# Optimization experiments

Measured on AMD Instinct MI355X. Metric: run time of the kernel, lower is better.

## Reference

```python
import jax, jax.numpy as jnp
import numpy as np

D_MODEL = 1024
N_HEADS = 16
D_K = D_MODEL // N_HEADS
LN_EPS = 1e-5


def setup_inputs() -> dict:
    key = jax.random.key(0)
    ks = jax.random.split(key, 8)
    B, Sq, Skv = 2, 2048, 2048
    scale = 1.0 / np.sqrt(D_MODEL)
    return {
        "query": jax.random.normal(ks[0], (B, Sq, D_MODEL), dtype=jnp.float32),
        "key_value": jax.random.normal(ks[1], (B, Skv, D_MODEL), dtype=jnp.float32),
        "W_qkv": jax.random.normal(ks[2], (3 * D_MODEL, D_MODEL), dtype=jnp.float32) * scale,
        "b_qkv": jax.random.normal(ks[3], (3 * D_MODEL,), dtype=jnp.float32) * 0.01,
        "W_o": jax.random.normal(ks[4], (D_MODEL, D_MODEL), dtype=jnp.float32) * scale,
        "b_o": jax.random.normal(ks[5], (D_MODEL,), dtype=jnp.float32) * 0.01,
        "ln_gamma": jnp.ones((D_MODEL,), dtype=jnp.float32),
        "ln_beta": jnp.zeros((D_MODEL,), dtype=jnp.float32),
    }


def _attention(query, key_value, W_qkv, b_qkv, W_o, b_o, ln_gamma, ln_beta):
    B, Sq, _ = query.shape
    Skv = key_value.shape[1]
    # Q from query rows of qkv_proj; K,V from key_value rows (slice weights -> same
    # math as projecting then slicing, without the discarded 2/3 and 1/3 compute).
    Wq, Wk, Wv = W_qkv[:D_MODEL], W_qkv[D_MODEL:2 * D_MODEL], W_qkv[2 * D_MODEL:]
    bq, bk, bv = b_qkv[:D_MODEL], b_qkv[D_MODEL:2 * D_MODEL], b_qkv[2 * D_MODEL:]
    Q = (query @ Wq.T + bq).reshape(B, Sq, N_HEADS, D_K).transpose(0, 2, 1, 3)
    K = (key_value @ Wk.T + bk).reshape(B, Skv, N_HEADS, D_K).transpose(0, 2, 1, 3)
    V = (key_value @ Wv.T + bv).reshape(B, Skv, N_HEADS, D_K).transpose(0, 2, 1, 3)
    # fp32 attention (original forces float32 inside autocast(enabled=False))
    scores = jnp.einsum('bhqd,bhkd->bhqk', Q.astype(jnp.float32), K.astype(jnp.float32))
    scores = scores / np.sqrt(D_K)
    attn = jax.nn.softmax(scores, axis=-1)  # dropout is identity at inference
    context = jnp.einsum('bhqk,bhkd->bhqd', attn, V.astype(jnp.float32)).astype(query.dtype)
    context = context.transpose(0, 2, 1, 3).reshape(B, Sq, D_MODEL)
    output = context @ W_o.T + b_o
    # residual + LayerNorm
    x = output + query
    mu = jnp.mean(x, axis=-1, keepdims=True)
    var = jnp.mean(jnp.square(x - mu), axis=-1, keepdims=True)
    return (x - mu) / jnp.sqrt(var + LN_EPS) * ln_gamma + ln_beta


def reference(query, key_value, W_qkv, b_qkv, W_o, b_o, ln_gamma, ln_beta):
    return _attention(query, key_value, W_qkv, b_qkv, W_o, b_o, ln_gamma, ln_beta)
```

## Files before the change

### kernel.cpp

```cpp
#include <hip/hip_runtime.h>
#include <hip/hip_bf16.h>

typedef __attribute__((ext_vector_type(4))) float f32x4;
typedef __attribute__((ext_vector_type(16))) float f32x16;
typedef __attribute__((ext_vector_type(8))) __bf16 bf16x8;
typedef __attribute__((ext_vector_type(2))) __bf16 bf16x2;

#define DEV __device__ __forceinline__

DEV unsigned short f2bf(float f) {
    union { float f; unsigned u; } x; x.f = f;
    unsigned r = x.u + 0x7fffu + ((x.u >> 16) & 1u);
    return (unsigned short)(r >> 16);
}

DEV unsigned packbf(float a, float b) {
    union { bf16x2 h; unsigned u; } t;
    t.h[0] = (__bf16)a; t.h[1] = (__bf16)b;
    return t.u;
}

DEV float bflo(unsigned u) { union { unsigned u; float f; } x; x.u = u << 16; return x.f; }
DEV float bfhi(unsigned u) { union { unsigned u; float f; } x; x.u = u & 0xffff0000u; return x.f; }

DEV void gload16(const void* g, void* l) {
    __builtin_amdgcn_global_load_lds(
        (const __attribute__((address_space(1))) void*)g,
        (__attribute__((address_space(3))) void*)l, 16, 0, 0);
}

#define PLSWAP(a, b) asm("v_permlane32_swap_b32 %0, %1" : "+v"(a), "+v"(b))

DEV bf16x8 ldsfrag(const unsigned short* base, int row, int kcol) {
    int byte = (row << 7) + (kcol << 1);
    byte ^= (row & 7) << 4;
    return *reinterpret_cast<const bf16x8*>(reinterpret_cast<const char*>(base) + byte);
}

__global__ __launch_bounds__(256) void cvt_all(
    const float* __restrict__ q, const float* __restrict__ kv,
    const float* __restrict__ wq, const float* __restrict__ wo,
    unsigned short* __restrict__ qb, unsigned short* __restrict__ kvb,
    unsigned short* __restrict__ wqb, unsigned short* __restrict__ wob)
{
    int i = blockIdx.x * 256 + threadIdx.x;
    const float* s; unsigned short* d; int o;
    if (i < 2097152) {
        if (i < 1048576) { s = q;  d = qb;  o = i; }
        else             { s = kv; d = kvb; o = i - 1048576; }
    } else {
        if (i < 2883584) { s = wq; d = wqb; o = i - 2097152; }
        else             { s = wo; d = wob; o = i - 2883584; }
    }
    f32x4 v = *reinterpret_cast<const f32x4*>(s + (size_t)o * 4);
    ushort4 u;
    u.x = f2bf(v.x); u.y = f2bf(v.y); u.z = f2bf(v.z); u.w = f2bf(v.w);
    *reinterpret_cast<ushort4*>(d + (size_t)o * 4) = u;
}

__global__ __launch_bounds__(256) void gemm_qkv(
    const unsigned short* __restrict__ Aq,
    const unsigned short* __restrict__ Akv,
    const unsigned short* __restrict__ W,
    const float* __restrict__ bias,
    unsigned short* __restrict__ QP,
    unsigned short* __restrict__ KP,
    unsigned short* __restrict__ VP)
{
    __shared__ unsigned short lA[2][128 * 64];
    __shared__ unsigned short lB[2][128 * 64];
    int bn = blockIdx.x % 24, bm = blockIdx.x / 24;
    int m0 = bm * 128, n0 = bn * 128;
    const unsigned short* A = (bn < 8) ? Aq : Akv;
    int tid = threadIdx.x, lane = tid & 63, wv = tid >> 6;
    int wm = (wv >> 1) * 64, wn = (wv & 1) * 64;
    int cg = lane >> 4, cl = lane & 15;

    const unsigned short* sA[4];
    const unsigned short* sB[4];
#pragma unroll
    for (int p = 0; p < 4; ++p) {
        int o = p * 4096 + tid * 16;
        int r = o >> 7;
        int c = ((o ^ ((r & 7) << 4)) >> 1) & 63;
        sA[p] = A + (size_t)(m0 + r) * 1024 + c;
        sB[p] = W + (size_t)(n0 + r) * 1024 + c;
    }
    const int dl = wv * 1024;

    auto STAGE = [&](int buf, int k0) {
#pragma unroll
        for (int p = 0; p < 4; ++p) {
            gload16(sA[p] + k0, (char*)lA[buf] + p * 4096 + dl);
            gload16(sB[p] + k0, (char*)lB[buf] + p * 4096 + dl);
        }
    };

    f32x4 acc[4][4] = {};

    STAGE(0, 0);
    for (int kt = 0; kt < 16; ++kt) {
        const int cur = kt & 1;
        if (kt < 15) {
            STAGE(cur ^ 1, (kt + 1) * 64);
            asm volatile("s_waitcnt vmcnt(8)" ::: "memory");
        } else {
            asm volatile("s_waitcnt vmcnt(0)" ::: "memory");
        }
        __builtin_amdgcn_s_barrier();
#pragma unroll
        for (int ks = 0; ks < 2; ++ks) {
            bf16x8 af[4], bfr[4];
#pragma unroll
            for (int i = 0; i < 4; ++i) af[i] = ldsfrag(lA[cur], wm + i * 16 + cl, ks * 32 + cg * 8);
#pragma unroll
            for (int j = 0; j < 4; ++j) bfr[j] = ldsfrag(lB[cur], wn + j * 16 + cl, ks * 32 + cg * 8);
#pragma unroll
            for (int i = 0; i < 4; ++i)
#pragma unroll
                for (int j = 0; j < 4; ++j)
                    acc[i][j] = __builtin_amdgcn_mfma_f32_16x16x32_bf16(af[i], bfr[j], acc[i][j], 0, 0, 0);
        }
        asm volatile("s_waitcnt lgkmcnt(0)" ::: "memory");
        __builtin_amdgcn_s_barrier();
    }

    unsigned short* img = (unsigned short*)lA;
    const int which = (bn >= 16) ? 2 : (bn >= 8 ? 1 : 0);
    const float scale = (which == 0) ? 0.18033688f : 1.0f;

#pragma unroll
    for (int j = 0; j < 4; ++j) {
        int nn = wn + j * 16 + cl;
        int d = nn & 63, chunk = nn >> 6;
        float bv = bias[n0 + nn];
#pragma unroll
        for (int i = 0; i < 4; ++i) {
#pragma unroll
            for (int r = 0; r < 4; ++r) {
                int mm = wm + i * 16 + cg * 4 + r;
                float v = (acc[i][j][r] + bv) * scale;
                int off;
                if (which < 2)
                    off = ((mm >> 5) * 4 + (d >> 4)) * 512
                        + (((d >> 3) & 1) * 32 + (mm & 31)) * 8 + (d & 7);
                else
                    off = (((mm >> 6) * 2 + (d >> 5)) * 4 + ((mm >> 4) & 3)) * 512
                        + (((mm >> 3) & 1) * 32 + (d & 31)) * 8 + (mm & 7);
                img[chunk * 8192 + off] = f2bf(v);
            }
        }
    }
    __syncthreads();

    int bb = m0 >> 11, s0 = m0 & 2047;
    int h0 = (bn & 7) * 2;
    unsigned short* dst[2];
#pragma unroll
    for (int c = 0; c < 2; ++c) {
        int bh = bb * 16 + h0 + c;
        if (which == 0)      dst[c] = QP + ((size_t)bh * 64 + (s0 >> 5)) * 2048;
        else if (which == 1) dst[c] = KP + ((size_t)bh * 64 + (s0 >> 5)) * 2048;
        else                 dst[c] = VP + ((size_t)bh * 32 + (s0 >> 6)) * 4096;
    }
#pragma unroll
    for (int c = 0; c < 2; ++c)
#pragma unroll
        for (int k = 0; k < 4; ++k) {
            int e = (k * 256 + tid) * 8;
            *reinterpret_cast<uint4*>(dst[c] + e) =
                *reinterpret_cast<const uint4*>(img + c * 8192 + e);
        }
}

__global__ __launch_bounds__(256, 2) void attn(
    const unsigned short* __restrict__ QP,
    const unsigned short* __restrict__ KP,
    const unsigned short* __restrict__ VP,
    unsigned short* __restrict__ OP,
    float2* __restrict__ ML)
{
    int swz = (blockIdx.x & 7) * 64 + (blockIdx.x >> 3);
    int bh = swz >> 4;
    int qc = (swz >> 1) & 7;
    int spl = swz & 1;
    int tid = threadIdx.x, lane = tid & 63, wv = tid >> 6;
    int ql = lane & 31, hh = lane >> 5;
    int qs = qc * 256 + wv * 64;
    const unsigned short* kp = KP + (size_t)bh * 131072 + lane * 8;
    const unsigned short* vp = VP + (size_t)bh * 131072 + lane * 8;
    const int tbase = spl * 16;

    bf16x8 qfA[4], qfB[4];
    {
        const unsigned short* qpA = QP + ((size_t)(bh * 64 + (qs >> 5)) * 4) * 512 + lane * 8;
#pragma unroll
        for (int ks = 0; ks < 4; ++ks) {
            qfA[ks] = *reinterpret_cast<const bf16x8*>(qpA + ks * 512);
            qfB[ks] = *reinterpret_cast<const bf16x8*>(qpA + 2048 + ks * 512);
        }
    }

    bf16x8 ka[4], kc[4], va[4], vc[4];
    auto LOADK = [&](int t) {
        const unsigned short* b = kp + (size_t)t * 4096;
#pragma unroll
        for (int ks = 0; ks < 4; ++ks) {
            ka[ks] = *reinterpret_cast<const bf16x8*>(b + ks * 512);
            kc[ks] = *reinterpret_cast<const bf16x8*>(b + 2048 + ks * 512);
        }
    };
    auto LOADV = [&](int t) {
        const unsigned short* b = vp + (size_t)t * 4096;
#pragma unroll
        for (int kh = 0; kh < 4; ++kh) {
            va[kh] = *reinterpret_cast<const bf16x8*>(b + kh * 512);
            vc[kh] = *reinterpret_cast<const bf16x8*>(b + 2048 + kh * 512);
        }
    };

    f32x16 oA0 = {}, oA1 = {}, oB0 = {}, oB1 = {};
    f32x4 psA = {0.f, 0.f, 0.f, 0.f}, psB = {0.f, 0.f, 0.f, 0.f};

    auto EXPPACK = [&](f32x16& s0, f32x16& s1, unsigned (&pb)[4][4], f32x4& psa) {
#pragma unroll
        for (int r = 0; r < 16; r += 4) {
            s0[r]     = __builtin_amdgcn_exp2f(s0[r]);     psa[0] += s0[r];
            s0[r + 1] = __builtin_amdgcn_exp2f(s0[r + 1]); psa[1] += s0[r + 1];
            s0[r + 2] = __builtin_amdgcn_exp2f(s0[r + 2]); psa[2] += s0[r + 2];
            s0[r + 3] = __builtin_amdgcn_exp2f(s0[r + 3]); psa[3] += s0[r + 3];
        }
#pragma unroll
        for (int r = 0; r < 16; r += 4) {
            s1[r]     = __builtin_amdgcn_exp2f(s1[r]);     psa[0] += s1[r];
            s1[r + 1] = __builtin_amdgcn_exp2f(s1[r + 1]); psa[1] += s1[r + 1];
            s1[r + 2] = __builtin_amdgcn_exp2f(s1[r + 2]); psa[2] += s1[r + 2];
            s1[r + 3] = __builtin_amdgcn_exp2f(s1[r + 3]); psa[3] += s1[r + 3];
        }
        unsigned A0 = packbf(s0[0], s0[1]),   B0 = packbf(s0[2], s0[3]);
        unsigned C0 = packbf(s0[4], s0[5]),   D0 = packbf(s0[6], s0[7]);
        unsigned E0 = packbf(s0[8], s0[9]),   F0 = packbf(s0[10], s0[11]);
        unsigned G0 = packbf(s0[12], s0[13]), H0 = packbf(s0[14], s0[15]);
        unsigned A1 = packbf(s1[0], s1[1]),   B1 = packbf(s1[2], s1[3]);
        unsigned C1 = packbf(s1[4], s1[5]),   D1 = packbf(s1[6], s1[7]);
        unsigned E1 = packbf(s1[8], s1[9]),   F1 = packbf(s1[10], s1[11]);
        unsigned G1 = packbf(s1[12], s1[13]), H1 = packbf(s1[14], s1[15]);
        PLSWAP(A0, C0); PLSWAP(B0, D0); PLSWAP(E0, G0); PLSWAP(F0, H0);
        PLSWAP(A1, C1); PLSWAP(B1, D1); PLSWAP(E1, G1); PLSWAP(F1, H1);
        pb[0][0] = A0; pb[0][1] = B0; pb[0][2] = C0; pb[0][3] = D0;
        pb[1][0] = E0; pb[1][1] = F0; pb[1][2] = G0; pb[1][3] = H0;
        pb[2][0] = A1; pb[2][1] = B1; pb[2][2] = C1; pb[2][3] = D1;
        pb[3][0] = E1; pb[3][1] = F1; pb[3][2] = G1; pb[3][3] = H1;
    };

    LOADK(tbase);
    LOADV(tbase);
    for (int t = 0; t < 16; ++t) {
        f32x16 sA0 = {}, sA1 = {};
        __builtin_amdgcn_s_setprio(1);
#pragma unroll
        for (int ks = 0; ks < 4; ++ks) {
            sA0 = __builtin_amdgcn_mfma_f32_32x32x16_bf16(ka[ks], qfA[ks], sA0, 0, 0, 0);
            sA1 = __builtin_amdgcn_mfma_f32_32x32x16_bf16(kc[ks], qfA[ks], sA1, 0, 0, 0);
        }
        __builtin_amdgcn_s_setprio(0);
        unsigned pbA[4][4];
        EXPPACK(sA0, sA1, pbA, psA);
        f32x16 sB0 = {}, sB1 = {};
        __builtin_amdgcn_s_setprio(1);
#pragma unroll
        for (int ks = 0; ks < 4; ++ks) {
            sB0 = __builtin_amdgcn_mfma_f32_32x32x16_bf16(ka[ks], qfB[ks], sB0, 0, 0, 0);
            sB1 = __builtin_amdgcn_mfma_f32_32x32x16_bf16(kc[ks], qfB[ks], sB1, 0, 0, 0);
        }
        __builtin_amdgcn_s_setprio(0);
        LOADK(tbase + t + 1);
        __builtin_amdgcn_s_setprio(1);
#pragma unroll
        for (int kh = 0; kh < 4; ++kh) {
            union { unsigned u[4]; bf16x8 v; } pa;
            pa.u[0] = pbA[kh][0]; pa.u[1] = pbA[kh][1];
            pa.u[2] = pbA[kh][2]; pa.u[3] = pbA[kh][3];
            oA0 = __builtin_amdgcn_mfma_f32_32x32x16_bf16(va[kh], pa.v, oA0, 0, 0, 0);
            oA1 = __builtin_amdgcn_mfma_f32_32x32x16_bf16(vc[kh], pa.v, oA1, 0, 0, 0);
        }
        __builtin_amdgcn_s_setprio(0);
        unsigned pbB[4][4];
        EXPPACK(sB0, sB1, pbB, psB);
        __builtin_amdgcn_s_setprio(1);
#pragma unroll
        for (int kh = 0; kh < 4; ++kh) {
            union { unsigned u[4]; bf16x8 v; } pc;
            pc.u[0] = pbB[kh][0]; pc.u[1] = pbB[kh][1];
            pc.u[2] = pbB[kh][2]; pc.u[3] = pbB[kh][3];
            oB0 = __builtin_amdgcn_mfma_f32_32x32x16_bf16(va[kh], pc.v, oB0, 0, 0, 0);
            oB1 = __builtin_amdgcn_mfma_f32_32x32x16_bf16(vc[kh], pc.v, oB1, 0, 0, 0);
        }
        __builtin_amdgcn_s_setprio(0);
        LOADV(tbase + t + 1);
    }

    float lA = (psA[0] + psA[1]) + (psA[2] + psA[3]);
    float lB = (psB[0] + psB[1]) + (psB[2] + psB[3]);
    float lAx = lA, lBx = lB;
    PLSWAP(lA, lAx); PLSWAP(lB, lBx);
    lA += lAx; lB += lBx;

    size_t rowA = (size_t)(spl * 32 + bh) * 2048 + qs + ql;
    size_t rowB = rowA + 32;
    if (hh == 0) {
        ML[rowA] = make_float2(0.0f, lA);
        ML[rowB] = make_float2(0.0f, lB);
    }
    float invA = 1.0f / lA, invB = 1.0f / lB;
    unsigned short* cpA = OP + rowA * 64 + hh * 4;
    unsigned short* cpB = OP + rowB * 64 + hh * 4;
#pragma unroll
    for (int m = 0; m < 4; ++m) {
        uint2 w0, w1;
        w0.x = packbf(oA0[4 * m] * invA, oA0[4 * m + 1] * invA);
        w0.y = packbf(oA0[4 * m + 2] * invA, oA0[4 * m + 3] * invA);
        w1.x = packbf(oA1[4 * m] * invA, oA1[4 * m + 1] * invA);
        w1.y = packbf(oA1[4 * m + 2] * invA, oA1[4 * m + 3] * invA);
        *reinterpret_cast<uint2*>(cpA + 8 * m) = w0;
        *reinterpret_cast<uint2*>(cpA + 32 + 8 * m) = w1;
        w0.x = packbf(oB0[4 * m] * invB, oB0[4 * m + 1] * invB);
        w0.y = packbf(oB0[4 * m + 2] * invB, oB0[4 * m + 3] * invB);
        w1.x = packbf(oB1[4 * m] * invB, oB1[4 * m + 1] * invB);
        w1.y = packbf(oB1[4 * m + 2] * invB, oB1[4 * m + 3] * invB);
        *reinterpret_cast<uint2*>(cpB + 8 * m) = w0;
        *reinterpret_cast<uint2*>(cpB + 32 + 8 * m) = w1;
    }
}

__global__ __launch_bounds__(256) void combine(
    const unsigned short* __restrict__ OP,
    const float2* __restrict__ ML,
    unsigned short* __restrict__ ctx)
{
    int row = blockIdx.x * 256 + threadIdx.x;
    int bh = row >> 11, q = row & 2047;
    float2 ml1 = ML[row];
    float2 ml2 = ML[65536 + row];
    float M = fmaxf(ml1.x, ml2.x);
    float w1 = ml1.y * __builtin_amdgcn_exp2f(ml1.x - M);
    float w2 = ml2.y * __builtin_amdgcn_exp2f(ml2.x - M);
    float inv = 1.0f / (w1 + w2);
    w1 *= inv; w2 *= inv;
    const unsigned short* p1 = OP + (size_t)row * 64;
    const unsigned short* p2 = OP + ((size_t)65536 + row) * 64;
    int b = bh >> 4, h = bh & 15;
    unsigned short* op = ctx + (size_t)(b * 2048 + q) * 1024 + h * 64;
#pragma unroll
    for (int c = 0; c < 8; ++c) {
        uint4 u1 = *reinterpret_cast<const uint4*>(p1 + c * 8);
        uint4 u2 = *reinterpret_cast<const uint4*>(p2 + c * 8);
        uint4 r;
        r.x = packbf(bflo(u1.x) * w1 + bflo(u2.x) * w2, bfhi(u1.x) * w1 + bfhi(u2.x) * w2);
        r.y = packbf(bflo(u1.y) * w1 + bflo(u2.y) * w2, bfhi(u1.y) * w1 + bfhi(u2.y) * w2);
        r.z = packbf(bflo(u1.z) * w1 + bflo(u2.z) * w2, bfhi(u1.z) * w1 + bfhi(u2.z) * w2);
        r.w = packbf(bflo(u1.w) * w1 + bflo(u2.w) * w2, bfhi(u1.w) * w1 + bfhi(u2.w) * w2);
        *reinterpret_cast<uint4*>(op + c * 8) = r;
    }
}

__global__ __launch_bounds__(256) void gemm_out(
    const unsigned short* __restrict__ A,
    const unsigned short* __restrict__ W,
    const float* __restrict__ bo,
    const float* __restrict__ resid,
    float* __restrict__ X)
{
    __shared__ unsigned short lA[3][64 * 64];
    __shared__ unsigned short lB[3][128 * 64];
    int bn = blockIdx.x & 7, bm = blockIdx.x >> 3;
    int m0 = bm * 64, n0 = bn * 128;
    int tid = threadIdx.x, lane = tid & 63, wv = tid >> 6;
    int wm = (wv >> 1) * 32, wn = (wv & 1) * 64;
    int cg = lane >> 4, cl = lane & 15;

    const unsigned short* sA[2];
    const unsigned short* sB[4];
#pragma unroll
    for (int p = 0; p < 2; ++p) {
        int o = p * 4096 + tid * 16;
        int r = o >> 7;
        int c = ((o ^ ((r & 7) << 4)) >> 1) & 63;
        sA[p] = A + (size_t)(m0 + r) * 1024 + c;
    }
#pragma unroll
    for (int p = 0; p < 4; ++p) {
        int o = p * 4096 + tid * 16;
        int r = o >> 7;
        int c = ((o ^ ((r & 7) << 4)) >> 1) & 63;
        sB[p] = W + (size_t)(n0 + r) * 1024 + c;
    }
    const int dl = wv * 1024;

    auto STAGE = [&](int buf, int k0) {
#pragma unroll
        for (int p = 0; p < 2; ++p)
            gload16(sA[p] + k0, (char*)lA[buf] + p * 4096 + dl);
#pragma unroll
        for (int p = 0; p < 4; ++p)
            gload16(sB[p] + k0, (char*)lB[buf] + p * 4096 + dl);
    };

    f32x4 acc[2][4] = {};

    STAGE(0, 0);
    STAGE(1, 64);
    int cur = 0;
    for (int kt = 0; kt < 16; ++kt) {
        __builtin_amdgcn_s_barrier();
        if (kt < 14) {
            int nb = (cur >= 1) ? cur - 1 : 2;
            STAGE(nb, (kt + 2) * 64);
            asm volatile("s_waitcnt vmcnt(12)" ::: "memory");
        } else if (kt == 14) {
            asm volatile("s_waitcnt vmcnt(6)" ::: "memory");
        } else {
            asm volatile("s_waitcnt vmcnt(0)" ::: "memory");
        }
#pragma unroll
        for (int ks = 0; ks < 2; ++ks) {
            bf16x8 af[2], bfr[4];
#pragma unroll
            for (int i = 0; i < 2; ++i) af[i] = ldsfrag(lA[cur], wm + i * 16 + cl, ks * 32 + cg * 8);
#pragma unroll
            for (int j = 0; j < 4; ++j) bfr[j] = ldsfrag(lB[cur], wn + j * 16 + cl, ks * 32 + cg * 8);
#pragma unroll
            for (int i = 0; i < 2; ++i)
#pragma unroll
                for (int j = 0; j < 4; ++j)
                    acc[i][j] = __builtin_amdgcn_mfma_f32_16x16x32_bf16(af[i], bfr[j], acc[i][j], 0, 0, 0);
        }
        cur = (cur == 2) ? 0 : cur + 1;
    }

#pragma unroll
    for (int j = 0; j < 4; ++j) {
        int n = n0 + wn + j * 16 + cl;
        float bv = bo[n];
#pragma unroll
        for (int i = 0; i < 2; ++i)
#pragma unroll
            for (int r = 0; r < 4; ++r) {
                int m = m0 + wm + i * 16 + cg * 4 + r;
                size_t idx = (size_t)m * 1024 + n;
                X[idx] = acc[i][j][r] + bv + resid[idx];
            }
    }
}

__global__ __launch_bounds__(256) void ln_k(float* __restrict__ X,
                                            const float* __restrict__ gam,
                                            const float* __restrict__ bet)
{
    __shared__ float red[8];
    int row = blockIdx.x, tid = threadIdx.x;
    int lane = tid & 63, wv = tid >> 6;
    f32x4 v = *reinterpret_cast<const f32x4*>(X + (size_t)row * 1024 + tid * 4);
    float s = (v.x + v.y) + (v.z + v.w);
#pragma unroll
    for (int m = 32; m >= 1; m >>= 1) s += __shfl_xor(s, m, 64);
    if (lane == 0) red[wv] = s;
    __syncthreads();
    float mu = (red[0] + red[1] + red[2] + red[3]) * (1.0f / 1024.0f);
    f32x4 d = v - mu;
    float sq = (d.x * d.x + d.y * d.y) + (d.z * d.z + d.w * d.w);
#pragma unroll
    for (int m = 32; m >= 1; m >>= 1) sq += __shfl_xor(sq, m, 64);
    if (lane == 0) red[4 + wv] = sq;
    __syncthreads();
    float var = (red[4] + red[5] + red[6] + red[7]) * (1.0f / 1024.0f);
    float rstd = rsqrtf(var + 1e-5f);
    f32x4 gg = *reinterpret_cast<const f32x4*>(gam + tid * 4);
    f32x4 bb = *reinterpret_cast<const f32x4*>(bet + tid * 4);
    f32x4 y;
    y.x = d.x * rstd * gg.x + bb.x;
    y.y = d.y * rstd * gg.y + bb.y;
    y.z = d.z * rstd * gg.z + bb.z;
    y.w = d.w * rstd * gg.w + bb.w;
    *reinterpret_cast<f32x4*>(X + (size_t)row * 1024 + tid * 4) = y;
}

extern "C" void kernel_launch(void* const* d_in, const int* in_sizes, int n_in,
                              void* d_out, int out_size, void* d_ws, size_t ws_size,
                              hipStream_t stream) {
    const float* query     = (const float*)d_in[0];
    const float* key_value = (const float*)d_in[1];
    const float* W_qkv     = (const float*)d_in[2];
    const float* b_qkv     = (const float*)d_in[3];
    const float* W_o       = (const float*)d_in[4];
    const float* b_o       = (const float*)d_in[5];
    const float* ln_gamma  = (const float*)d_in[6];
    const float* ln_beta   = (const float*)d_in[7];
    float* out = (float*)d_out;

    char* ws = (char*)d_ws;
    const size_t MB = 1u << 20;
    unsigned short* qb   = (unsigned short*)(ws + 0 * MB);
    unsigned short* kvb  = (unsigned short*)(ws + 8 * MB);
    unsigned short* wqb  = (unsigned short*)(ws + 16 * MB);
    unsigned short* wob  = (unsigned short*)(ws + 22 * MB);
    unsigned short* QP   = (unsigned short*)(ws + 24 * MB);
    unsigned short* KP   = (unsigned short*)(ws + 32 * MB);
    unsigned short* VP   = (unsigned short*)(ws + 40 * MB);
    unsigned short* ctx  = (unsigned short*)(ws + 48 * MB);
    unsigned short* OP   = (unsigned short*)(ws + 0 * MB);
    float2*         ML   = (float2*)(ws + 20 * MB);

    (void)in_sizes; (void)n_in; (void)out_size; (void)ws_size;

    cvt_all<<<12288, 256, 0, stream>>>(query, key_value, W_qkv, W_o, qb, kvb, wqb, wob);

    gemm_qkv<<<32 * 24, 256, 0, stream>>>(qb, kvb, wqb, b_qkv, QP, KP, VP);
    attn<<<512, 256, 0, stream>>>(QP, KP, VP, OP, ML);
    combine<<<256, 256, 0, stream>>>(OP, ML, ctx);
    gemm_out<<<512, 256, 0, stream>>>(ctx, wob, b_o, query, out);
    ln_k<<<4096, 256, 0, stream>>>(out, ln_gamma, ln_beta);
}
```

Before: 133.9 us.

## Triple-buffer QKV GEMM with K=32 tiles and fragment-ordered LDS layout

The QKV projection GEMM moves from a double-buffered 64-wide K tile to a triple-buffered 32-wide K tile, prefetching two stages ahead with one barrier per iteration. The LDS layout now stores each tile in MFMA-fragment order, so every lane reads its operand with a single contiguous 16-byte load instead of swizzled addressing. LDS use drops to 48KB and launch bounds ask for three blocks per CU to raise occupancy. The trade-off is twice as many loop iterations and barriers, plus possible register pressure from the occupancy hint.

```diff
diff --git a/kernel.cpp b/kernel.cpp
--- a/kernel.cpp
+++ b/kernel.cpp
@@ -58,7 +58,7 @@
     *reinterpret_cast<ushort4*>(d + (size_t)o * 4) = u;
 }
 
-__global__ __launch_bounds__(256) void gemm_qkv(
+__global__ __launch_bounds__(256, 3) void gemm_qkv(
     const unsigned short* __restrict__ Aq,
     const unsigned short* __restrict__ Akv,
     const unsigned short* __restrict__ W,
@@ -67,67 +67,69 @@
     unsigned short* __restrict__ KP,
     unsigned short* __restrict__ VP)
 {
-    __shared__ unsigned short lA[2][128 * 64];
-    __shared__ unsigned short lB[2][128 * 64];
+    __shared__ unsigned short lds[24576];
     int bn = blockIdx.x % 24, bm = blockIdx.x / 24;
     int m0 = bm * 128, n0 = bn * 128;
     const unsigned short* A = (bn < 8) ? Aq : Akv;
     int tid = threadIdx.x, lane = tid & 63, wv = tid >> 6;
-    int wm = (wv >> 1) * 64, wn = (wv & 1) * 64;
     int cg = lane >> 4, cl = lane & 15;
 
-    const unsigned short* sA[4];
-    const unsigned short* sB[4];
-#pragma unroll
-    for (int p = 0; p < 4; ++p) {
-        int o = p * 4096 + tid * 16;
-        int r = o >> 7;
-        int c = ((o ^ ((r & 7) << 4)) >> 1) & 63;
-        sA[p] = A + (size_t)(m0 + r) * 1024 + c;
-        sB[p] = W + (size_t)(n0 + r) * 1024 + c;
-    }
+    const unsigned short* sA[2];
+    const unsigned short* sB[2];
+#pragma unroll
+    for (int p = 0; p < 2; ++p) {
+        int row = (p * 4 + wv) * 16 + cl;
+        sA[p] = A + (size_t)(m0 + row) * 1024 + cg * 8;
+        sB[p] = W + (size_t)(n0 + row) * 1024 + cg * 8;
+    }
+    char* lbase = (char*)lds;
     const int dl = wv * 1024;
 
-    auto STAGE = [&](int buf, int k0) {
-#pragma unroll
-        for (int p = 0; p < 4; ++p) {
-            gload16(sA[p] + k0, (char*)lA[buf] + p * 4096 + dl);
-            gload16(sB[p] + k0, (char*)lB[buf] + p * 4096 + dl);
+    auto STAGE = [&](int buf, int kt) {
+        const int k0 = kt * 32;
+#pragma unroll
+        for (int p = 0; p < 2; ++p) {
+            gload16(sA[p] + k0, lbase + buf * 8192 + p * 4096 + dl);
+            gload16(sB[p] + k0, lbase + 24576 + buf * 8192 + p * 4096 + dl);
         }
     };
 
     f32x4 acc[4][4] = {};
 
     STAGE(0, 0);
-    for (int kt = 0; kt < 16; ++kt) {
-        const int cur = kt & 1;
-        if (kt < 15) {
-            STAGE(cur ^ 1, (kt + 1) * 64);
+    STAGE(1, 1);
+    int cur = 0;
+    for (int kt = 0; kt < 32; ++kt) {
+        __builtin_amdgcn_s_barrier();
+        if (kt < 30) {
+            int nb = (cur >= 1) ? cur - 1 : 2;
+            STAGE(nb, kt + 2);
             asm volatile("s_waitcnt vmcnt(8)" ::: "memory");
+        } else if (kt == 30) {
+            asm volatile("s_waitcnt vmcnt(4)" ::: "memory");
         } else {
             asm volatile("s_waitcnt vmcnt(0)" ::: "memory");
         }
-        __builtin_amdgcn_s_barrier();
-#pragma unroll
-        for (int ks = 0; ks < 2; ++ks) {
-            bf16x8 af[4], bfr[4];
-#pragma unroll
-            for (int i = 0; i < 4; ++i) af[i] = ldsfrag(lA[cur], wm + i * 16 + cl, ks * 32 + cg * 8);
-#pragma unroll
-            for (int j = 0; j < 4; ++j) bfr[j] = ldsfrag(lB[cur], wn + j * 16 + cl, ks * 32 + cg * 8);
-#pragma unroll
-            for (int i = 0; i < 4; ++i)
-#pragma unroll
-                for (int j = 0; j < 4; ++j)
-                    acc[i][j] = __builtin_amdgcn_mfma_f32_16x16x32_bf16(af[i], bfr[j], acc[i][j], 0, 0, 0);
-        }
-        asm volatile("s_waitcnt lgkmcnt(0)" ::: "memory");
-        __builtin_amdgcn_s_barrier();
-    }
-
-    unsigned short* img = (unsigned short*)lA;
+        const unsigned short* au = lds + cur * 4096 + ((wv >> 1) * 4) * 512 + lane * 8;
+        const unsigned short* bu = lds + 12288 + cur * 4096 + ((wv & 1) * 4) * 512 + lane * 8;
+        bf16x8 af[4], bfr[4];
+#pragma unroll
+        for (int i = 0; i < 4; ++i) af[i] = *reinterpret_cast<const bf16x8*>(au + i * 512);
+#pragma unroll
+        for (int j = 0; j < 4; ++j) bfr[j] = *reinterpret_cast<const bf16x8*>(bu + j * 512);
+#pragma unroll
+        for (int i = 0; i < 4; ++i)
+#pragma unroll
+            for (int j = 0; j < 4; ++j)
+                acc[i][j] = __builtin_amdgcn_mfma_f32_16x16x32_bf16(af[i], bfr[j], acc[i][j], 0, 0, 0);
+        cur = (cur == 2) ? 0 : cur + 1;
+    }
+    __syncthreads();
+
+    unsigned short* img = (unsigned short*)lds;
     const int which = (bn >= 16) ? 2 : (bn >= 8 ? 1 : 0);
     const float scale = (which == 0) ? 0.18033688f : 1.0f;
+    const int wm = (wv >> 1) * 64, wn = (wv & 1) * 64;
 
 #pragma unroll
     for (int j = 0; j < 4; ++j) {
```

Result: slower. 138.2 us (+3.2%).
